# Kernel optimization log

Hardware: AMD Instinct MI355X
Metric: run time of the kernel (lower is better)

Reference implementation:

```python
import jax, jax.numpy as jnp
import numpy as np

BS, N_AGENTS, SA_DIM, HID = 2048, 64, 128, 256


def setup_inputs() -> dict:
    key = jax.random.key(0)
    ks = jax.random.split(key, 16)
    s = lambda fan_in: 1.0 / np.sqrt(fan_in)
    u = lambda k, shp, b: jax.random.uniform(k, shp, jnp.float32, -b, b)
    return {
        "x": jax.random.normal(ks[0], (BS, N_AGENTS, SA_DIM), jnp.float32),
        # encoder: Linear(sa, hid) -> Linear(hid, hid)
        "enc_w1": u(ks[1], (SA_DIM, HID), s(SA_DIM)),
        "enc_b1": u(ks[2], (HID,), s(SA_DIM)),
        "enc_w2": u(ks[3], (HID, HID), s(HID)),
        "enc_b2": u(ks[4], (HID,), s(HID)),
        # attention 'general' linear_in (no bias)
        "attn_w": u(ks[5], (HID, HID), s(HID)),
        # gc1: Linear(sa, hid); nn_gc1: Linear(sa, hid)
        "gc1_w": u(ks[6], (SA_DIM, HID), s(SA_DIM)),
        "gc1_b": u(ks[7], (HID,), s(SA_DIM)),
        "nn1_w": u(ks[8], (SA_DIM, HID), s(SA_DIM)),
        "nn1_b": u(ks[9], (HID,), s(SA_DIM)),
        # gc2: Linear(hid, hid); nn_gc2: Linear(hid, hid)
        "gc2_w": u(ks[10], (HID, HID), s(HID)),
        "gc2_b": u(ks[11], (HID,), s(HID)),
        "nn2_w": u(ks[12], (HID, HID), s(HID)),
        "nn2_b": u(ks[13], (HID,), s(HID)),
        "n_agents": N_AGENTS,
    }


def reference(x, enc_w1, enc_b1, enc_w2, enc_b2, attn_w,
              gc1_w, gc1_b, nn1_w, nn1_b, gc2_w, gc2_b, nn2_w, nn2_b,
              n_agents):
    relu = jax.nn.relu
    inv_n = 1.0 / n_agents
    # encoder MLP: relu(relu(x W1 + b1) W2 + b2)  -> [bs, n, hid]
    emb = relu(relu(x @ enc_w1 + enc_b1) @ enc_w2 + enc_b2)
    # general attention: softmax((emb W_a) emb^T) over last axis -> [bs, n, n]
    scores = jnp.einsum('bnd,bmd->bnm', emb @ attn_w, emb)
    attn = jax.nn.softmax(scores, axis=-1)
    # gc1: adj @ Linear(x); residual relu branch; normalize by n_agents
    feat = relu(jnp.einsum('bnm,bmh->bnh', attn, x @ gc1_w + gc1_b))
    feat = (feat + relu(x @ nn1_w + nn1_b)) * inv_n
    # gc2 on feat
    out = relu(jnp.einsum('bnm,bmh->bnh', attn, feat @ gc2_w + gc2_b))
    out = (out + relu(feat @ nn2_w + nn2_b)) * inv_n
    return out, attn
```

## Files before the change

kernel.cpp:

```cpp
#include <hip/hip_runtime.h>

typedef _Float16 half8 __attribute__((ext_vector_type(8)));
typedef _Float16 half4_t __attribute__((ext_vector_type(4)));
typedef float f32x4 __attribute__((ext_vector_type(4)));

#define NBATCH 2048
#define NA 64
#define SA 128
#define HID 256

#define OFF_X 0
#define OFF_R0 8192
#define OFF_ATT (8192 + 16384)
#define SMEM_BYTES ((8192 + 16384 + 8192) * 2)

#define W_ENC1 0
#define W_ENC2 (W_ENC1 + 128 * 256)
#define W_ATTN (W_ENC2 + 256 * 256)
#define W_GC1 (W_ATTN + 256 * 256)
#define W_NN1 (W_GC1 + 128 * 256)
#define W_GC2 (W_NN1 + 128 * 256)
#define W_NN2 (W_GC2 + 256 * 256)

#define MFMA(a, b, cacc) __builtin_amdgcn_mfma_f32_16x16x32_f16((a), (b), (cacc), 0, 0, 0)

#define BAR()                                            \
  do {                                                   \
    asm volatile("s_waitcnt lgkmcnt(0)" ::: "memory");   \
    __builtin_amdgcn_s_barrier();                        \
  } while (0)

__global__ void pack_all(const float* __restrict__ e1, const float* __restrict__ e2,
                         const float* __restrict__ aw, const float* __restrict__ g1,
                         const float* __restrict__ n1, const float* __restrict__ g2,
                         const float* __restrict__ n2, _Float16* __restrict__ dst) {
  int b = (int)blockIdx.x;
  const float* src;
  int off;
  if (b < 16) { src = e1; off = W_ENC1; }
  else if (b < 48) { src = e2; off = W_ENC2; b -= 16; }
  else if (b < 80) { src = aw; off = W_ATTN; b -= 48; }
  else if (b < 96) { src = g1; off = W_GC1; b -= 80; }
  else if (b < 112) { src = n1; off = W_NN1; b -= 96; }
  else if (b < 144) { src = g2; off = W_GC2; b -= 112; }
  else { src = n2; off = W_NN2; b -= 144; }
  int t = b * 256 + (int)threadIdx.x;
  int lane = t & 63, frag = t >> 6;
  int nt = frag & 15, kt = frag >> 4;
  int g = lane >> 4, c = lane & 15;
  half8 h;
#pragma unroll
  for (int j = 0; j < 8; ++j)
    h[j] = (_Float16)src[(size_t)(kt * 32 + g * 8 + j) * 256 + nt * 16 + c];
  *(half8*)(dst + off + (size_t)t * 8) = h;
}

__global__ __launch_bounds__(256, 2) void dicg_main(
    const float* __restrict__ x, const float* __restrict__ b_enc1,
    const float* __restrict__ b_enc2, const float* __restrict__ b_gc1,
    const float* __restrict__ b_nn1, const float* __restrict__ b_gc2,
    const float* __restrict__ b_nn2, const _Float16* __restrict__ wp,
    float* __restrict__ out, float* __restrict__ attn_out) {
  extern __shared__ _Float16 sm[];
  _Float16* X = sm + OFF_X;
  _Float16* R0 = sm + OFF_R0;
  _Float16* ATTp = sm + OFF_ATT;

  const int tid = (int)threadIdx.x;
  const int wv = tid >> 6;
  const int lane = tid & 63;
  const int g = lane >> 4;
  const int c = lane & 15;
  const int bb = (int)blockIdx.x;
  const float* __restrict__ xb = x + (size_t)bb * (NA * SA);

  auto ldA = [&](const _Float16* p, int kt, int rt) -> half8 {
    return *(const half8*)(p + (kt * 4 + rt) * 512 + lane * 8);
  };
  auto ldB = [&](const _Float16* p, int kt, int ct) -> half8 {
    return *(const half8*)(p + (kt * 16 + ct) * 512 + lane * 8);
  };
  auto ldFeat = [&](int kt, int rt) -> half8 {
    return *(const half8*)(R0 + ((kt & 1) * 16 + 4 * (kt >> 1) + rt) * 512 + lane * 8);
  };
  auto wfrag = [&](const _Float16* wb, int kt, int ntg) -> half8 {
    return *(const half8*)(wb + ((size_t)(kt * 16 + ntg) * 64 + lane) * 8);
  };
  auto xfrag = [&](int r0, int k0) -> half8 {
    const float* p = xb + (r0 + c) * SA + k0 + g * 8;
    f32x4 u = *(const f32x4*)p;
    f32x4 v = *(const f32x4*)(p + 4);
    half8 h;
    h[0] = (_Float16)u[0]; h[1] = (_Float16)u[1];
    h[2] = (_Float16)u[2]; h[3] = (_Float16)u[3];
    h[4] = (_Float16)v[0]; h[5] = (_Float16)v[1];
    h[6] = (_Float16)v[2]; h[7] = (_Float16)v[3];
    return h;
  };

  auto stA_val = [&](_Float16* dst, int rt, int nt, int r, float v) {
    int kt = 2 * wv + (nt >> 1);
    int lanep = (2 * (nt & 1) + (c >> 3)) * 16 + 4 * g + r;
    dst[(kt * 4 + rt) * 512 + lanep * 8 + (c & 7)] = (_Float16)v;
  };
  auto ep_storeA = [&](f32x4(&acc)[4][4], const float* bias, bool dorelu) {
#pragma unroll
    for (int nt = 0; nt < 4; ++nt) {
      float bv = bias[64 * wv + 16 * nt + c];
#pragma unroll
      for (int rt = 0; rt < 4; ++rt)
#pragma unroll
        for (int r = 0; r < 4; ++r) {
          float y = acc[rt][nt][r] + bv;
          if (dorelu) y = fmaxf(y, 0.f);
          stA_val(R0, rt, nt, r, y);
        }
    }
  };
  auto ep_storeB = [&](f32x4(&acc)[4][4], const float* bias) {
#pragma unroll
    for (int nt = 0; nt < 4; ++nt) {
      float bv = bias[64 * wv + 16 * nt + c];
#pragma unroll
      for (int rt = 0; rt < 4; ++rt) {
        half4_t h;
#pragma unroll
        for (int r = 0; r < 4; ++r) h[r] = (_Float16)(acc[rt][nt][r] + bv);
        int fi = (rt >> 1) * 16 + 4 * wv + nt;
        int lanep = (2 * (rt & 1) + (g >> 1)) * 16 + c;
        *(half4_t*)(R0 + fi * 512 + lanep * 8 + 4 * (g & 1)) = h;
      }
    }
  };
  auto stFeatT = [&](int nt, int rt, half4_t hv) {
    int fi = (nt >> 1) * 16 + 4 * wv + rt;
    int lanep = (2 * (nt & 1) + (g >> 1)) * 16 + c;
    *(half4_t*)(R0 + fi * 512 + lanep * 8 + 4 * (g & 1)) = hv;
  };
  auto stQ = [&](const f32x4(&q2)[2], int s) {
    _Float16* base = ATTp + (8 + 2 * wv + s) * 512;
#pragma unroll
    for (int nt2 = 0; nt2 < 2; ++nt2)
#pragma unroll
      for (int r = 0; r < 4; ++r)
        base[((2 * nt2 + (c >> 3)) * 16 + 4 * g + r) * 8 + (c & 7)] = (_Float16)q2[nt2][r];
  };

  half8 pf2[4][4];
  half8 pfq[8][2];
  half8 pf5g[2][4], pf5n[2][4];
  half8 pf7n[3][4], pf7g[3][4];

  {
    f32x4 acc[4][4]{};
#pragma unroll
    for (int kt = 0; kt < 4; ++kt) {
      half8 af[4], bf[4];
#pragma unroll
      for (int rt = 0; rt < 4; ++rt) af[rt] = xfrag(16 * rt, kt * 32);
#pragma unroll
      for (int nt = 0; nt < 4; ++nt) bf[nt] = wfrag(wp + W_ENC1, kt, 4 * wv + nt);
      if (kt == wv) {
#pragma unroll
        for (int rt = 0; rt < 4; ++rt)
          *(half8*)(X + (kt * 4 + rt) * 512 + lane * 8) = af[rt];
      }
#pragma unroll
      for (int rt = 0; rt < 4; ++rt)
#pragma unroll
        for (int nt = 0; nt < 4; ++nt) acc[rt][nt] = MFMA(af[rt], bf[nt], acc[rt][nt]);
    }
#pragma unroll
    for (int s = 0; s < 4; ++s)
#pragma unroll
      for (int nt = 0; nt < 4; ++nt) pf2[s][nt] = wfrag(wp + W_ENC2, s, 4 * wv + nt);
    ep_storeA(acc, b_enc1, true);
  }
  BAR();
  {
    f32x4 acc[4][4]{};
#pragma unroll
    for (int kt = 0; kt < 8; ++kt) {
      half8 af[4], bf[4];
#pragma unroll
      for (int rt = 0; rt < 4; ++rt) af[rt] = ldA(R0, kt, rt);
#pragma unroll
      for (int nt = 0; nt < 4; ++nt)
        bf[nt] = (kt < 4) ? pf2[kt][nt] : wfrag(wp + W_ENC2, kt, 4 * wv + nt);
#pragma unroll
      for (int rt = 0; rt < 4; ++rt)
#pragma unroll
        for (int nt = 0; nt < 4; ++nt) acc[rt][nt] = MFMA(af[rt], bf[nt], acc[rt][nt]);
    }
#pragma unroll
    for (int k2 = 0; k2 < 8; ++k2) {
      pfq[k2][0] = wfrag(wp + W_ATTN, k2, 0);
      pfq[k2][1] = wfrag(wp + W_ATTN, k2, 1);
    }
    BAR();
    ep_storeA(acc, b_enc2, true);
  }
  BAR();
  {
    half8 aeK[8];
#pragma unroll
    for (int k2 = 0; k2 < 8; ++k2) aeK[k2] = ldA(R0, k2, wv);
    f32x4 sc[4]{};
    {
      f32x4 q2[2]{};
#pragma unroll
      for (int k2 = 0; k2 < 8; ++k2) {
        q2[0] = MFMA(aeK[k2], pfq[k2][0], q2[0]);
        q2[1] = MFMA(aeK[k2], pfq[k2][1], q2[1]);
      }
      stQ(q2, 0);
    }
#pragma unroll
    for (int ktp = 0; ktp < 8; ++ktp) {
      f32x4 q2n[2]{};
      if (ktp < 7) {
#pragma unroll
        for (int k2 = 0; k2 < 8; ++k2) {
          q2n[0] = MFMA(aeK[k2], wfrag(wp + W_ATTN, k2, 2 * ktp + 2), q2n[0]);
          q2n[1] = MFMA(aeK[k2], wfrag(wp + W_ATTN, k2, 2 * ktp + 3), q2n[1]);
        }
      }
      asm volatile("s_waitcnt lgkmcnt(0)" ::: "memory");
      half8 qb = *(const half8*)(ATTp + (8 + 2 * wv + (ktp & 1)) * 512 + lane * 8);
      if (ktp < 7) stQ(q2n, (ktp + 1) & 1);
#pragma unroll
      for (int rt = 0; rt < 4; ++rt) sc[rt] = MFMA(ldA(R0, ktp, rt), qb, sc[rt]);
    }
    float m = sc[0][0];
#pragma unroll
    for (int rt = 0; rt < 4; ++rt)
#pragma unroll
      for (int r = 0; r < 4; ++r) m = fmaxf(m, sc[rt][r]);
    m = fmaxf(m, __shfl_xor(m, 16));
    m = fmaxf(m, __shfl_xor(m, 32));
    float e[4][4], s = 0.f;
#pragma unroll
    for (int rt = 0; rt < 4; ++rt)
#pragma unroll
      for (int r = 0; r < 4; ++r) {
        e[rt][r] = __expf(sc[rt][r] - m);
        s += e[rt][r];
      }
    s += __shfl_xor(s, 16);
    s += __shfl_xor(s, 32);
    float inv = 1.0f / s;
#pragma unroll
    for (int s5 = 0; s5 < 2; ++s5)
#pragma unroll
      for (int nt = 0; nt < 4; ++nt) {
        pf5g[s5][nt] = wfrag(wp + W_GC1, s5, 4 * wv + nt);
        pf5n[s5][nt] = wfrag(wp + W_NN1, s5, 4 * wv + nt);
      }
    float* ao = attn_out + ((size_t)bb * NA + 16 * wv + c) * NA;
#pragma unroll
    for (int rt = 0; rt < 4; ++rt) {
      f32x4 vv;
      half4_t hh;
#pragma unroll
      for (int r = 0; r < 4; ++r) {
        vv[r] = e[rt][r] * inv;
        hh[r] = (_Float16)vv[r];
      }
      *(f32x4*)(ao + 16 * rt + 4 * g) = vv;
      int fi = (rt >> 1) * 4 + wv;
      int lanep = (2 * (rt & 1) + (g >> 1)) * 16 + c;
      *(half4_t*)(ATTp + fi * 512 + lanep * 8 + 4 * (g & 1)) = hh;
    }
  }
  BAR();
  half4_t r1h[4][4];
  {
    f32x4 aG[4][4]{}, aN[4][4]{};
#pragma unroll
    for (int kt = 0; kt < 4; ++kt) {
      half8 af[4], b1[4], b2[4];
#pragma unroll
      for (int rt = 0; rt < 4; ++rt) af[rt] = ldA(X, kt, rt);
#pragma unroll
      for (int nt = 0; nt < 4; ++nt)
        b1[nt] = (kt < 2) ? pf5g[kt][nt] : wfrag(wp + W_GC1, kt, 4 * wv + nt);
#pragma unroll
      for (int nt = 0; nt < 4; ++nt)
        b2[nt] = (kt < 2) ? pf5n[kt][nt] : wfrag(wp + W_NN1, kt, 4 * wv + nt);
#pragma unroll
      for (int rt = 0; rt < 4; ++rt)
#pragma unroll
        for (int nt = 0; nt < 4; ++nt) {
          aG[rt][nt] = MFMA(af[rt], b1[nt], aG[rt][nt]);
          aN[nt][rt] = MFMA(b2[nt], af[rt], aN[nt][rt]);
        }
    }
    ep_storeB(aG, b_gc1);
#pragma unroll
    for (int nt = 0; nt < 4; ++nt) {
      f32x4 bv4 = *(const f32x4*)(b_nn1 + 64 * wv + 16 * nt + 4 * g);
#pragma unroll
      for (int rt = 0; rt < 4; ++rt)
#pragma unroll
        for (int r = 0; r < 4; ++r)
          r1h[nt][rt][r] = (_Float16)fmaxf(aN[nt][rt][r] + bv4[r], 0.f);
    }
#pragma unroll
    for (int s2 = 0; s2 < 2; ++s2)
#pragma unroll
      for (int nt = 0; nt < 4; ++nt) {
        pf7n[s2][nt] = wfrag(wp + W_NN2, s2, 4 * wv + nt);
        pf7g[s2][nt] = wfrag(wp + W_GC2, s2, 4 * wv + nt);
      }
  }
  {
#pragma unroll
    for (int nt = 0; nt < 4; ++nt) {
      pf7n[2][nt] = wfrag(wp + W_NN2, 2, 4 * wv + nt);
      pf7g[2][nt] = wfrag(wp + W_GC2, 2, 4 * wv + nt);
    }
    f32x4 a1[4][4]{};
#pragma unroll
    for (int kt = 0; kt < 2; ++kt) {
      half8 af[4], bf[4];
#pragma unroll
      for (int rt = 0; rt < 4; ++rt) af[rt] = ldA(ATTp, kt, rt);
#pragma unroll
      for (int nt = 0; nt < 4; ++nt) bf[nt] = ldB(R0, kt, 4 * wv + nt);
#pragma unroll
      for (int rt = 0; rt < 4; ++rt)
#pragma unroll
        for (int nt = 0; nt < 4; ++nt) a1[nt][rt] = MFMA(bf[nt], af[rt], a1[nt][rt]);
    }
#pragma unroll
    for (int nt = 0; nt < 4; ++nt)
#pragma unroll
      for (int rt = 0; rt < 4; ++rt) {
        half4_t hv;
#pragma unroll
        for (int r = 0; r < 4; ++r)
          hv[r] = (_Float16)((fmaxf(a1[nt][rt][r], 0.f) + (float)r1h[nt][rt][r]) *
                             0.015625f);
        stFeatT(nt, rt, hv);
      }
  }
  BAR();
  half4_t r2h[4][4];
  {
    f32x4 aN2[4][4]{}, aG2[4][4]{};
#pragma unroll
    for (int kt = 0; kt < 8; ++kt) {
      half8 af[4], b1[4], b2[4];
#pragma unroll
      for (int rt = 0; rt < 4; ++rt) af[rt] = ldFeat(kt, rt);
#pragma unroll
      for (int nt = 0; nt < 4; ++nt)
        b1[nt] = (kt < 3) ? pf7n[kt][nt] : wfrag(wp + W_NN2, kt, 4 * wv + nt);
#pragma unroll
      for (int nt = 0; nt < 4; ++nt)
        b2[nt] = (kt < 3) ? pf7g[kt][nt] : wfrag(wp + W_GC2, kt, 4 * wv + nt);
#pragma unroll
      for (int rt = 0; rt < 4; ++rt)
#pragma unroll
        for (int nt = 0; nt < 4; ++nt) {
          aN2[nt][rt] = MFMA(b1[nt], af[rt], aN2[nt][rt]);
          aG2[rt][nt] = MFMA(af[rt], b2[nt], aG2[rt][nt]);
        }
    }
#pragma unroll
    for (int nt = 0; nt < 4; ++nt) {
      f32x4 bv4 = *(const f32x4*)(b_nn2 + 64 * wv + 16 * nt + 4 * g);
#pragma unroll
      for (int rt = 0; rt < 4; ++rt)
#pragma unroll
        for (int r = 0; r < 4; ++r)
          r2h[nt][rt][r] = (_Float16)fmaxf(aN2[nt][rt][r] + bv4[r], 0.f);
    }
    BAR();
    ep_storeB(aG2, b_gc2);
  }
  {
    f32x4 a1[4][4]{};
#pragma unroll
    for (int kt = 0; kt < 2; ++kt) {
      half8 af[4], bf[4];
#pragma unroll
      for (int rt = 0; rt < 4; ++rt) af[rt] = ldA(ATTp, kt, rt);
#pragma unroll
      for (int nt = 0; nt < 4; ++nt) bf[nt] = ldB(R0, kt, 4 * wv + nt);
#pragma unroll
      for (int rt = 0; rt < 4; ++rt)
#pragma unroll
        for (int nt = 0; nt < 4; ++nt) a1[nt][rt] = MFMA(bf[nt], af[rt], a1[nt][rt]);
    }
    float* ob = out + (size_t)bb * NA * HID;
#pragma unroll
    for (int nt = 0; nt < 4; ++nt)
#pragma unroll
      for (int rt = 0; rt < 4; ++rt) {
        f32x4 vv;
#pragma unroll
        for (int r = 0; r < 4; ++r)
          vv[r] = (fmaxf(a1[nt][rt][r], 0.f) + (float)r2h[nt][rt][r]) * 0.015625f;
        *(f32x4*)(ob + (size_t)(16 * rt + c) * HID + 64 * wv + 16 * nt + 4 * g) = vv;
      }
  }
}

extern "C" void kernel_launch(void* const* d_in, const int* in_sizes, int n_in,
                              void* d_out, int out_size, void* d_ws, size_t ws_size,
                              hipStream_t stream) {
  const float* x = (const float*)d_in[0];
  const float* enc_w1 = (const float*)d_in[1];
  const float* enc_b1 = (const float*)d_in[2];
  const float* enc_w2 = (const float*)d_in[3];
  const float* enc_b2 = (const float*)d_in[4];
  const float* attn_w = (const float*)d_in[5];
  const float* gc1_w = (const float*)d_in[6];
  const float* gc1_b = (const float*)d_in[7];
  const float* nn1_w = (const float*)d_in[8];
  const float* nn1_b = (const float*)d_in[9];
  const float* gc2_w = (const float*)d_in[10];
  const float* gc2_b = (const float*)d_in[11];
  const float* nn2_w = (const float*)d_in[12];
  const float* nn2_b = (const float*)d_in[13];

  _Float16* wp = (_Float16*)d_ws;
  float* out = (float*)d_out;
  float* attn_o = out + (size_t)NBATCH * NA * HID;

  pack_all<<<176, 256, 0, stream>>>(enc_w1, enc_w2, attn_w, gc1_w, nn1_w, gc2_w,
                                    nn2_w, wp);
  dicg_main<<<NBATCH, 256, SMEM_BYTES, stream>>>(
      x, enc_b1, enc_b2, gc1_b, nn1_b, gc2_b, nn2_b, wp, out, attn_o);
}
```

Measured before the change: 156.3 us.

## Keep x fragments in registers instead of LDS, shrink shared memory footprint

The x tile's half-precision fragments stay in registers (xr) from the first GEMM through the gc1/nn1 stage instead of being staged through a shared-memory X buffer. This cuts LDS from 64KB to 40KB and repacks the Q ping-pong slots at the start of the attention region. To free registers it drops the prefetched attention weights and gc1/nn1 weights and halves the enc2 prefetch, so those weights now load from global memory at point of use. The aim is lower LDS use, possibly more resident blocks, and fewer LDS round trips, at the cost of extra register pressure and exposed global-load latency.

```diff
diff --git a/kernel.cpp b/kernel.cpp
--- a/kernel.cpp
+++ b/kernel.cpp
@@ -9,10 +9,9 @@
 #define SA 128
 #define HID 256
 
-#define OFF_X 0
-#define OFF_R0 8192
-#define OFF_ATT (8192 + 16384)
-#define SMEM_BYTES ((8192 + 16384 + 8192) * 2)
+#define OFF_R0 0
+#define OFF_ATT 16384
+#define SMEM_BYTES 40960
 
 #define W_ENC1 0
 #define W_ENC2 (W_ENC1 + 128 * 256)
@@ -62,7 +61,6 @@
     const float* __restrict__ b_nn2, const _Float16* __restrict__ wp,
     float* __restrict__ out, float* __restrict__ attn_out) {
   extern __shared__ _Float16 sm[];
-  _Float16* X = sm + OFF_X;
   _Float16* R0 = sm + OFF_R0;
   _Float16* ATTp = sm + OFF_ATT;
 
@@ -138,7 +136,7 @@
     *(half4_t*)(R0 + fi * 512 + lanep * 8 + 4 * (g & 1)) = hv;
   };
   auto stQ = [&](const f32x4(&q2)[2], int s) {
-    _Float16* base = ATTp + (8 + 2 * wv + s) * 512;
+    _Float16* base = ATTp + (wv + 4 * s) * 512;
 #pragma unroll
     for (int nt2 = 0; nt2 < 2; ++nt2)
 #pragma unroll
@@ -146,32 +144,26 @@
         base[((2 * nt2 + (c >> 3)) * 16 + 4 * g + r) * 8 + (c & 7)] = (_Float16)q2[nt2][r];
   };
 
-  half8 pf2[4][4];
-  half8 pfq[8][2];
-  half8 pf5g[2][4], pf5n[2][4];
+  half8 xr[4][4];
+  half8 pf2[2][4];
   half8 pf7n[3][4], pf7g[3][4];
 
   {
     f32x4 acc[4][4]{};
 #pragma unroll
     for (int kt = 0; kt < 4; ++kt) {
-      half8 af[4], bf[4];
-#pragma unroll
-      for (int rt = 0; rt < 4; ++rt) af[rt] = xfrag(16 * rt, kt * 32);
+      half8 bf[4];
+#pragma unroll
+      for (int rt = 0; rt < 4; ++rt) xr[kt][rt] = xfrag(16 * rt, kt * 32);
 #pragma unroll
       for (int nt = 0; nt < 4; ++nt) bf[nt] = wfrag(wp + W_ENC1, kt, 4 * wv + nt);
-      if (kt == wv) {
-#pragma unroll
-        for (int rt = 0; rt < 4; ++rt)
-          *(half8*)(X + (kt * 4 + rt) * 512 + lane * 8) = af[rt];
-      }
-#pragma unroll
-      for (int rt = 0; rt < 4; ++rt)
-#pragma unroll
-        for (int nt = 0; nt < 4; ++nt) acc[rt][nt] = MFMA(af[rt], bf[nt], acc[rt][nt]);
-    }
-#pragma unroll
-    for (int s = 0; s < 4; ++s)
+#pragma unroll
+      for (int rt = 0; rt < 4; ++rt)
+#pragma unroll
+        for (int nt = 0; nt < 4; ++nt) acc[rt][nt] = MFMA(xr[kt][rt], bf[nt], acc[rt][nt]);
+    }
+#pragma unroll
+    for (int s = 0; s < 2; ++s)
 #pragma unroll
       for (int nt = 0; nt < 4; ++nt) pf2[s][nt] = wfrag(wp + W_ENC2, s, 4 * wv + nt);
     ep_storeA(acc, b_enc1, true);
@@ -186,16 +178,11 @@
       for (int rt = 0; rt < 4; ++rt) af[rt] = ldA(R0, kt, rt);
 #pragma unroll
       for (int nt = 0; nt < 4; ++nt)
-        bf[nt] = (kt < 4) ? pf2[kt][nt] : wfrag(wp + W_ENC2, kt, 4 * wv + nt);
+        bf[nt] = (kt < 2) ? pf2[kt][nt] : wfrag(wp + W_ENC2, kt, 4 * wv + nt);
 #pragma unroll
       for (int rt = 0; rt < 4; ++rt)
 #pragma unroll
         for (int nt = 0; nt < 4; ++nt) acc[rt][nt] = MFMA(af[rt], bf[nt], acc[rt][nt]);
-    }
-#pragma unroll
-    for (int k2 = 0; k2 < 8; ++k2) {
-      pfq[k2][0] = wfrag(wp + W_ATTN, k2, 0);
-      pfq[k2][1] = wfrag(wp + W_ATTN, k2, 1);
     }
     BAR();
     ep_storeA(acc, b_enc2, true);
@@ -210,8 +197,8 @@
       f32x4 q2[2]{};
 #pragma unroll
       for (int k2 = 0; k2 < 8; ++k2) {
-        q2[0] = MFMA(aeK[k2], pfq[k2][0], q2[0]);
-        q2[1] = MFMA(aeK[k2], pfq[k2][1], q2[1]);
+        q2[0] = MFMA(aeK[k2], wfrag(wp + W_ATTN, k2, 0), q2[0]);
+        q2[1] = MFMA(aeK[k2], wfrag(wp + W_ATTN, k2, 1), q2[1]);
       }
       stQ(q2, 0);
     }
@@ -226,7 +213,7 @@
         }
       }
       asm volatile("s_waitcnt lgkmcnt(0)" ::: "memory");
-      half8 qb = *(const half8*)(ATTp + (8 + 2 * wv + (ktp & 1)) * 512 + lane * 8);
+      half8 qb = *(const half8*)(ATTp + (wv + 4 * (ktp & 1)) * 512 + lane * 8);
       if (ktp < 7) stQ(q2n, (ktp + 1) & 1);
 #pragma unroll
       for (int rt = 0; rt < 4; ++rt) sc[rt] = MFMA(ldA(R0, ktp, rt), qb, sc[rt]);
@@ -249,13 +236,6 @@
     s += __shfl_xor(s, 16);
     s += __shfl_xor(s, 32);
     float inv = 1.0f / s;
-#pragma unroll
-    for (int s5 = 0; s5 < 2; ++s5)
-#pragma unroll
-      for (int nt = 0; nt < 4; ++nt) {
-        pf5g[s5][nt] = wfrag(wp + W_GC1, s5, 4 * wv + nt);
-        pf5n[s5][nt] = wfrag(wp + W_NN1, s5, 4 * wv + nt);
-      }
     float* ao = attn_out + ((size_t)bb * NA + 16 * wv + c) * NA;
 #pragma unroll
     for (int rt = 0; rt < 4; ++rt) {
@@ -278,21 +258,17 @@
     f32x4 aG[4][4]{}, aN[4][4]{};
 #pragma unroll
     for (int kt = 0; kt < 4; ++kt) {
-      half8 af[4], b1[4], b2[4];
-#pragma unroll
-      for (int rt = 0; rt < 4; ++rt) af[rt] = ldA(X, kt, rt);
-#pragma unroll
-      for (int nt = 0; nt < 4; ++nt)
-        b1[nt] = (kt < 2) ? pf5g[kt][nt] : wfrag(wp + W_GC1, kt, 4 * wv + nt);
-#pragma unroll
-      for (int nt = 0; nt < 4; ++nt)
-        b2[nt] = (kt < 2) ? pf5n[kt][nt] : wfrag(wp + W_NN1, kt, 4 * wv + nt);
+      half8 b1[4], b2[4];
+#pragma unroll
+      for (int nt = 0; nt < 4; ++nt) b1[nt] = wfrag(wp + W_GC1, kt, 4 * wv + nt);
+#pragma unroll
+      for (int nt = 0; nt < 4; ++nt) b2[nt] = wfrag(wp + W_NN1, kt, 4 * wv + nt);
 #pragma unroll
       for (int rt = 0; rt < 4; ++rt)
 #pragma unroll
         for (int nt = 0; nt < 4; ++nt) {
-          aG[rt][nt] = MFMA(af[rt], b1[nt], aG[rt][nt]);
-          aN[nt][rt] = MFMA(b2[nt], af[rt], aN[nt][rt]);
+          aG[rt][nt] = MFMA(xr[kt][rt], b1[nt], aG[rt][nt]);
+          aN[nt][rt] = MFMA(b2[nt], xr[kt][rt], aN[nt][rt]);
         }
     }
     ep_storeB(aG, b_gc1);
```

Result: slower. 159.7 us (+2.1%).
